# Kernel optimization log

Hardware: AMD Instinct MI355X
Metric: run time of the kernel (lower is better)

Reference implementation:

```python
import jax, jax.numpy as jnp
import numpy as np

K = 2  # kernel_size == stride (non-overlapping pool)

def setup_inputs() -> dict:
    key = jax.random.key(0)
    x = jax.random.normal(key, (32, 128, 128, 128), dtype=jnp.float32)
    return {"x": x}

def reference(x) -> jnp.ndarray:
    B, C, H, W = x.shape
    h, w = H // K, W // K
    # extract non-overlapping KxK patches: [B,C,h,w,K*K], row-major within window
    p = x.reshape(B, C, h, K, w, K).transpose(0, 1, 2, 4, 3, 5).reshape(B, C, h, w, K * K)
    vals = jnp.max(p, axis=-1)            # pooled values [B,C,h,w]
    idx = jnp.argmax(p, axis=-1)          # in-window flat index (first max, like torch)
    # decode global position of the max element
    row = jnp.arange(h, dtype=jnp.int32)[:, None] * K + (idx // K)  # [B,C,h,w]
    col = jnp.arange(w, dtype=jnp.int32)[None, :] * K + (idx % K)
    pos_h = row.astype(x.dtype) / H
    pos_w = col.astype(x.dtype) / W
    return jnp.concatenate([vals, pos_h, pos_w], axis=1)  # [B, 3C, h, w]
```

## Files before the change

### kernel.cpp

```cpp
#include <hip/hip_runtime.h>


__global__ __launch_bounds__(256) void pap_kernel(const float* __restrict__ x,
                                                  float* __restrict__ out) {
    constexpr int C = 128, H = 128, W = 128;
    constexpr int OH = 64, OW = 64;
    constexpr int OWP = OW / 2;
    constexpr int total = 32 * C * OH * OWP;
    constexpr float invH = 1.0f / (float)H;
    constexpr float invW = 1.0f / (float)W;

    for (int t = blockIdx.x * blockDim.x + threadIdx.x; t < total;
         t += gridDim.x * blockDim.x) {
        const int owp = t & (OWP - 1);
        const int oh  = (t >> 5) & (OH - 1);
        const int bc  = t >> 11;
        const int c   = bc & (C - 1);
        const int b   = bc >> 7;

        const size_t rowbase = ((size_t)bc * H + 2 * oh) * W + 4 * owp;
        const float4 r0 = *reinterpret_cast<const float4*>(x + rowbase);
        const float4 r1 = *reinterpret_cast<const float4*>(x + rowbase + W);

        float2 vals, ph, pw;
        {
            float v = r0.x; int idx = 0;
            if (r0.y > v) { v = r0.y; idx = 1; }
            if (r1.x > v) { v = r1.x; idx = 2; }
            if (r1.y > v) { v = r1.y; idx = 3; }
            vals.x = v;
            ph.x = (float)(2 * oh + (idx >> 1)) * invH;
            pw.x = (float)(4 * owp + (idx & 1)) * invW;
        }
        {
            float v = r0.z; int idx = 0;
            if (r0.w > v) { v = r0.w; idx = 1; }
            if (r1.z > v) { v = r1.z; idx = 2; }
            if (r1.w > v) { v = r1.w; idx = 3; }
            vals.y = v;
            ph.y = (float)(2 * oh + (idx >> 1)) * invH;
            pw.y = (float)(4 * owp + 2 + (idx & 1)) * invW;
        }

        const size_t plane = (size_t)C * OH * OW;
        const size_t obase = (((size_t)b * (3 * C) + c) * OH + oh) * OW + 2 * owp;
        *reinterpret_cast<float2*>(out + obase)             = vals;
        *reinterpret_cast<float2*>(out + obase + plane)     = ph;
        *reinterpret_cast<float2*>(out + obase + 2 * plane) = pw;
    }
}

extern "C" void kernel_launch(void* const* d_in, const int* in_sizes, int n_in,
                              void* d_out, int out_size, void* d_ws, size_t ws_size,
                              hipStream_t stream) {
    const float* x = (const float*)d_in[0];
    float* out = (float*)d_out;
    const int blocks = 2048;
    pap_kernel<<<blocks, 256, 0, stream>>>(x, out);
}
```

Baseline: 93.69 us.

## Use wave-per-tile contiguous row loads with cross-half shuffles and nontemporal I/O

```diff
diff --git a/kernel.cpp b/kernel.cpp
--- a/kernel.cpp
+++ b/kernel.cpp
@@ -1,52 +1,67 @@
 #include <hip/hip_runtime.h>
 
+
+typedef float f32x4 __attribute__((ext_vector_type(4)));
+typedef float f32x2 __attribute__((ext_vector_type(2)));
 
 __global__ __launch_bounds__(256) void pap_kernel(const float* __restrict__ x,
                                                   float* __restrict__ out) {
     constexpr int C = 128, H = 128, W = 128;
     constexpr int OH = 64, OW = 64;
-    constexpr int OWP = OW / 2;
-    constexpr int total = 32 * C * OH * OWP;
-    constexpr float invH = 1.0f / (float)H;
-    constexpr float invW = 1.0f / (float)W;
+    constexpr float inv = 1.0f / 128.0f;
+    constexpr int NTILES = 32 * C * (OH / 2);
+    constexpr size_t plane = (size_t)C * OH * OW;
 
-    for (int t = blockIdx.x * blockDim.x + threadIdx.x; t < total;
-         t += gridDim.x * blockDim.x) {
-        const int owp = t & (OWP - 1);
-        const int oh  = (t >> 5) & (OH - 1);
-        const int bc  = t >> 11;
-        const int c   = bc & (C - 1);
-        const int b   = bc >> 7;
+    const int lane = threadIdx.x & 63;
+    const int wid  = (blockIdx.x * blockDim.x + threadIdx.x) >> 6;
+    const int nw   = (gridDim.x * blockDim.x) >> 6;
+    const bool hi  = lane >= 32;
+    const int j    = lane & 31;
 
-        const size_t rowbase = ((size_t)bc * H + 2 * oh) * W + 4 * owp;
-        const float4 r0 = *reinterpret_cast<const float4*>(x + rowbase);
-        const float4 r1 = *reinterpret_cast<const float4*>(x + rowbase + W);
+    for (int t = wid; t < NTILES; t += nw) {
+        const int oh01 = t & 31;
+        const int bc   = t >> 5;
 
-        float2 vals, ph, pw;
+        const size_t base = (size_t)bc * (H * W) + (size_t)oh01 * (4 * W) + lane * 4;
+        f32x4 la = __builtin_nontemporal_load(reinterpret_cast<const f32x4*>(x + base));
+        f32x4 lb = __builtin_nontemporal_load(reinterpret_cast<const f32x4*>(x + base + 2 * W));
+
+        float top[4], bot[4];
+        #pragma unroll
+        for (int k = 0; k < 4; ++k) {
+            const float sa = __shfl_xor(la[k], 32, 64);
+            const float sb = __shfl_xor(lb[k], 32, 64);
+            top[k] = hi ? sb : la[k];
+            bot[k] = hi ? lb[k] : sa;
+        }
+
+        const int oh_out = 2 * oh01 + (hi ? 1 : 0);
+        f32x2 vals, ph, pw;
         {
-            float v = r0.x; int idx = 0;
-            if (r0.y > v) { v = r0.y; idx = 1; }
-            if (r1.x > v) { v = r1.x; idx = 2; }
-            if (r1.y > v) { v = r1.y; idx = 3; }
+            float v = top[0]; int idx = 0;
+            if (top[1] > v) { v = top[1]; idx = 1; }
+            if (bot[0] > v) { v = bot[0]; idx = 2; }
+            if (bot[1] > v) { v = bot[1]; idx = 3; }
             vals.x = v;
-            ph.x = (float)(2 * oh + (idx >> 1)) * invH;
-            pw.x = (float)(4 * owp + (idx & 1)) * invW;
+            ph.x = (float)(2 * oh_out + (idx >> 1)) * inv;
+            pw.x = (float)(4 * j + (idx & 1)) * inv;
         }
         {
-            float v = r0.z; int idx = 0;
-            if (r0.w > v) { v = r0.w; idx = 1; }
-            if (r1.z > v) { v = r1.z; idx = 2; }
-            if (r1.w > v) { v = r1.w; idx = 3; }
+            float v = top[2]; int idx = 0;
+            if (top[3] > v) { v = top[3]; idx = 1; }
+            if (bot[2] > v) { v = bot[2]; idx = 2; }
+            if (bot[3] > v) { v = bot[3]; idx = 3; }
             vals.y = v;
-            ph.y = (float)(2 * oh + (idx >> 1)) * invH;
-            pw.y = (float)(4 * owp + 2 + (idx & 1)) * invW;
+            ph.y = (float)(2 * oh_out + (idx >> 1)) * inv;
+            pw.y = (float)(4 * j + 2 + (idx & 1)) * inv;
         }
 
-        const size_t plane = (size_t)C * OH * OW;
-        const size_t obase = (((size_t)b * (3 * C) + c) * OH + oh) * OW + 2 * owp;
-        *reinterpret_cast<float2*>(out + obase)             = vals;
-        *reinterpret_cast<float2*>(out + obase + plane)     = ph;
-        *reinterpret_cast<float2*>(out + obase + 2 * plane) = pw;
+        const int b_ = bc >> 7, c = bc & (C - 1);
+        const size_t orow = ((size_t)(b_ * (3 * C) + c)) * (OH * OW)
+                          + (size_t)oh_out * OW + 2 * j;
+        __builtin_nontemporal_store(vals, reinterpret_cast<f32x2*>(out + orow));
+        __builtin_nontemporal_store(ph,   reinterpret_cast<f32x2*>(out + orow + plane));
+        __builtin_nontemporal_store(pw,   reinterpret_cast<f32x2*>(out + orow + 2 * plane));
     }
 }
 
@@ -55,6 +70,6 @@
                               hipStream_t stream) {
     const float* x = (const float*)d_in[0];
     float* out = (float*)d_out;
-    const int blocks = 2048;
+    const int blocks = 4096;
     pap_kernel<<<blocks, 256, 0, stream>>>(x, out);
 }
```

New measurement: 82.76 us. 1.13x faster.
